# Kernel optimization log

Measured on AMD Instinct MI355X. Metric: run time of the kernel, lower is better.

Reference implementation:

```python
import jax, jax.numpy as jnp
import numpy as np
from jax.scipy.special import digamma, gammaln

B, N, H, W, D = 16, 1024, 32, 32, 256
TEMP = 0.5
KL_WEIGHT = 1e-3


def setup_inputs() -> dict:
    key = jax.random.key(0)
    k1, k2, k3 = jax.random.split(key, 3)
    logits = jax.random.normal(k1, (B, N, H, W), dtype=jnp.float32)
    # codebook initialized uniform(-1/N, 1/N) as in init_type == 'uniform'
    codebook = jax.random.uniform(k2, (N, D), dtype=jnp.float32,
                                  minval=-1.0 / N, maxval=1.0 / N)
    # uniform noise for the Gumbel-softmax rsample (channels-last layout [B,H,W,N])
    uniform_noise = jax.random.uniform(k3, (B, H, W, N), dtype=jnp.float32,
                                       minval=1e-6, maxval=1.0 - 1e-6)
    return {"logits": logits, "codebook": codebook, "uniform_noise": uniform_noise}


def reference(logits, codebook, uniform_noise):
    # convert_to_alpha: evidential mapping alpha = softplus(logits) + 1,
    # then permute(0,2,3,1) -> [B, H, W, N]
    alpha = jax.nn.softplus(jnp.transpose(logits, (0, 2, 3, 1))) + 1.0
    S = jnp.sum(alpha, axis=-1, keepdims=True)            # [B,H,W,1]
    probs = alpha / S                                      # [B,H,W,N]

    # RelaxedOneHotCategorical(temp, probs).rsample() == Gumbel-softmax
    gumbel = -jnp.log(-jnp.log(uniform_noise))
    sample = jax.nn.softmax((jnp.log(probs) + gumbel) / TEMP, axis=-1)  # [B,H,W,N]

    vector_weights = jnp.transpose(sample, (0, 3, 1, 2))   # [B,N,H,W]
    indices = jnp.argmax(vector_weights, axis=1)           # [B,H,W]

    # quantized output via codebook combine
    z_q = jnp.einsum('bnhw,nd->bdhw', vector_weights, codebook)  # [B,D,H,W]

    # KL( Dirichlet(alpha) || Dirichlet(ones(N)) ), closed form with beta=1:
    # lgamma(S) - sum lgamma(alpha) - lgamma(N) + sum (alpha-1)*(digamma(alpha)-digamma(S))
    S1 = S[..., 0]
    kl = (gammaln(S1)
          - jnp.sum(gammaln(alpha), axis=-1)
          - gammaln(jnp.float32(N))
          + jnp.sum((alpha - 1.0) * (digamma(alpha) - digamma(S)), axis=-1))
    kl_loss = KL_WEIGHT * jnp.mean(kl)

    # perplexity over soft encodings
    avg_probs = jnp.mean(sample.reshape(-1, N), axis=0)
    perplexity = jnp.exp(-jnp.sum(avg_probs * jnp.log(avg_probs + 1e-10)))

    return (z_q, kl_loss, indices, perplexity)
```

## Files before the change

### kernel.cpp

```cpp
#include <hip/hip_runtime.h>
#include <math.h>

#define NB 16
#define NN 1024
#define NH 32
#define NW 32
#define ND 256
#define NPIX (NB*NH*NW)

#define ZQ_OFF  0
#define KL_OFF  4194304
#define IDX_OFF 4194305
#define PPL_OFF 4210689

#define LGAMMA_1024F 6071.2804f
#define BS_ROW_B 2080

typedef _Float16 f16x8 __attribute__((ext_vector_type(8)));
typedef _Float16 f16x4 __attribute__((ext_vector_type(4)));
typedef float    f32x4 __attribute__((ext_vector_type(4)));

__device__ __forceinline__ float fast_rcp(float x){ return __builtin_amdgcn_rcpf(x); }

__device__ __forceinline__ void lgamma_digamma(float a, float& lg, float& dg){
    float a1 = a + 1.f, a2 = a + 2.f, z = a + 3.f;
    float t12  = a1*a2;
    float prod = a*t12;
    float rz = fast_rcp(z);
    float rp = fast_rcp(prod);
    float lz = __logf(z);
    float lp = __logf(prod);
    float rz2 = rz*rz;
    lg = (z - 0.5f)*lz - z + 0.918938533f
       + rz*(0.083333333f - 0.002777778f*rz2) - lp;
    float sr = (t12 + a*(a + a + 3.f))*rp;
    dg = lz - 0.5f*rz - rz2*(0.083333333f - 0.008333333f*rz2) - sr;
}

__device__ __forceinline__ float elem(float x, float u,
                                      float& S, float& L, float& P){
    float t  = __expf(-fabsf(x));
    float a  = fmaxf(x, 0.f) + __logf(1.f + t) + 1.f;
    float lg, dg;
    lgamma_digamma(a, lg, dg);
    S += a; L += lg; P += (a - 1.f)*dg;
    float d = 1.f - u;
    float lup = -d*(1.f + d*(0.5f + d*(0.33333333f + d*(0.25f
              + d*(0.2f + d*(0.16666667f + d*0.14285714f))))));
    float lu = (d < 0.09f) ? lup : __logf(u);
    float ar = a * fast_rcp(lu);
    return ar*ar;
}

__global__ __launch_bounds__(256) void k_tr(
    const float* __restrict__ cb, _Float16* __restrict__ cbT)
{
    const int kb = blockIdx.x, kq = blockIdx.y, d = threadIdx.x;
    _Float16 tmp[8];
#pragma unroll
    for (int i = 0; i < 8; ++i)
        tmp[i] = (_Float16)cb[(size_t)(32*kb + 8*kq + i)*ND + d];
    *(f16x8*)(cbT + (size_t)kb*8192 + (size_t)d*32 + 8*kq) = *(f16x8*)tmp;
}

__global__ __launch_bounds__(1024, 2) void k_mega(
    const float* __restrict__ logits, const float* __restrict__ noise,
    const _Float16* __restrict__ cbT, float* __restrict__ colpart,
    float* __restrict__ klpart, float* __restrict__ out)
{
    __shared__ __align__(16) char lds[16*BS_ROW_B + 6*256*4];
    char*  bsb  = lds;
    float* redS = (float*)(lds + 16*BS_ROW_B);
    float* redL = redS + 256;
    float* redP = redL + 256;
    float* redZ = redP + 256;
    float* redM = redZ + 256;
    int*   redI = (int*)(redM + 256);

    const int t    = threadIdx.x;
    const int row  = blockIdx.x >> 1;
    const int w0   = (blockIdx.x & 1) * 16;
    const int b    = row >> 5, h = row & 31;
    const int lane = t & 63;
    const int v    = t >> 6;
    const int wl   = lane & 15;
    const int j4   = (lane >> 4) & 3;
    const int p    = row*32 + w0 + wl;
    const int nq   = 4*v + j4;

    const float* lgB = logits + (size_t)b*(NN*NH*NW) + (size_t)(4*nq)*(NH*NW)
                     + (size_t)h*NW + w0 + wl;
    const float* nzB = noise  + (size_t)p*NN + 4*nq;

    f32x4 u0, u1, u2, u3;
    float x00,x01,x02,x03, x10,x11,x12,x13;
    float x20,x21,x22,x23, x30,x31,x32,x33;
    float ev[16];
    float Sa = 0.f, La = 0.f, Pa = 0.f, Za = 0.f;
    float Sb = 0.f, Lb = 0.f, Pb = 0.f, Zb = 0.f;
    float mxA = -1.f, mxB = -1.f;
    int   idxA = 0, idxB = 0;

    asm volatile(
        "global_load_dwordx4 %0, %4, off\n\t"
        "global_load_dwordx4 %1, %4, off offset:1024\n\t"
        "global_load_dwordx4 %2, %4, off offset:2048\n\t"
        "global_load_dwordx4 %3, %4, off offset:3072"
        : "=&v"(u0), "=&v"(u1), "=&v"(u2), "=&v"(u3)
        : "v"(nzB));

#define LG_ASM(X0,X1,X2,X3,KK) \
    asm volatile( \
        "global_load_dword %0, %4, off offset:-4096\n\t" \
        "global_load_dword %1, %4, off\n\t" \
        "global_load_dword %2, %5, off offset:-4096\n\t" \
        "global_load_dword %3, %5, off" \
        : "=&v"(X0), "=&v"(X1), "=&v"(X2), "=&v"(X3) \
        : "v"(lgB + (size_t)(256*(KK))*1024 + 1024), \
          "v"(lgB + (size_t)(256*(KK))*1024 + 3072))

    LG_ASM(x00,x01,x02,x03, 0);
    LG_ASM(x10,x11,x12,x13, 1);
    LG_ASM(x20,x21,x22,x23, 2);
    LG_ASM(x30,x31,x32,x33, 3);
#undef LG_ASM

#define WAITV(NSTR) do{ asm volatile("s_waitcnt vmcnt(" NSTR ")"); \
                        __builtin_amdgcn_sched_barrier(0); }while(0)

#define DO_EA(kk,mm,X,UC) do{                                     \
    float e = elem(X, UC, Sa, La, Pa);                            \
    Za += e;                                                      \
    if (e > mxA){ mxA = e; idxA = 256*(kk) + 4*nq + (mm); }       \
    ev[4*(kk)+(mm)] = e; }while(0)

#define DO_EB(kk,mm,X,UC) do{                                     \
    float e = elem(X, UC, Sb, Lb, Pb);                            \
    Zb += e;                                                      \
    if (e > mxB){ mxB = e; idxB = 256*(kk) + 4*nq + (mm); }       \
    ev[4*(kk)+(mm)] = e; }while(0)

    WAITV("12");
    DO_EA(0,0,x00,u0[0]); DO_EB(0,1,x01,u0[1]);
    DO_EA(0,2,x02,u0[2]); DO_EB(0,3,x03,u0[3]);
    WAITV("8");
    DO_EA(1,0,x10,u1[0]); DO_EB(1,1,x11,u1[1]);
    DO_EA(1,2,x12,u1[2]); DO_EB(1,3,x13,u1[3]);
    WAITV("4");
    DO_EA(2,0,x20,u2[0]); DO_EB(2,1,x21,u2[1]);
    DO_EA(2,2,x22,u2[2]); DO_EB(2,3,x23,u2[3]);
    WAITV("0");
    DO_EA(3,0,x30,u3[0]); DO_EB(3,1,x31,u3[1]);
    DO_EA(3,2,x32,u3[2]); DO_EB(3,3,x33,u3[3]);
#undef WAITV
#undef DO_EA
#undef DO_EB

    float S = Sa + Sb, L = La + Lb, P = Pa + Pb, Z = Za + Zb;
    float mx; int idx;
    {
        bool take = (mxB > mxA) || (mxB == mxA && idxB < idxA);
        mx  = take ? mxB : mxA;
        idx = take ? idxB : idxA;
    }

#pragma unroll
    for (int mask = 16; mask < 64; mask <<= 1){
        S += __shfl_xor(S, mask);
        L += __shfl_xor(L, mask);
        P += __shfl_xor(P, mask);
        Z += __shfl_xor(Z, mask);
        float mo = __shfl_xor(mx, mask);
        int   io = __shfl_xor(idx, mask);
        bool take = (mo > mx) || (mo == mx && io < idx);
        mx  = take ? mo : mx;
        idx = take ? io : idx;
    }
    if (j4 == 0){
        redS[16*v + wl] = S;  redL[16*v + wl] = L;
        redP[16*v + wl] = P;  redZ[16*v + wl] = Z;
        redM[16*v + wl] = mx; redI[16*v + wl] = idx;
    }
    __syncthreads();

    float Zt = 0.f;
#pragma unroll
    for (int qz = 0; qz < 16; ++qz) Zt += redZ[16*qz + wl];
    const float zinv = fast_rcp(Zt);

    {
        char* brow = bsb + wl*BS_ROW_B;
        const int sw   = wl & 7;
        const int sub8 = (nq & 1) << 3;
        const int cb2  = nq >> 1;
#pragma unroll
        for (int k = 0; k < 4; ++k){
            f16x4 hv;
            hv[0] = (_Float16)(ev[4*k+0]*zinv);
            hv[1] = (_Float16)(ev[4*k+1]*zinv);
            hv[2] = (_Float16)(ev[4*k+2]*zinv);
            hv[3] = (_Float16)(ev[4*k+3]*zinv);
            *(f16x4*)(brow + (((32*k + cb2) ^ sw) << 4) + sub8) = hv;
        }
    }
    __syncthreads();

    const _Float16* aBase = cbT + (size_t)(16*v + wl)*32 + j4*8;
    const char* bRow = bsb + wl*BS_ROW_B;
    const int fsw = wl & 7;

    f32x4 acc = (f32x4)0.f;
    f16x8 ar[4];
    ar[0] = *(const f16x8*)(aBase);
    ar[1] = *(const f16x8*)(aBase + 8192);
    ar[2] = *(const f16x8*)(aBase + 2*8192);
    __builtin_amdgcn_sched_barrier(0);

#pragma unroll
    for (int kb = 0; kb < 32; ++kb){
        if (kb + 3 < 32){
            ar[(kb+3)&3] = *(const f16x8*)(aBase + (size_t)(kb+3)*8192);
            __builtin_amdgcn_sched_barrier(0);
        }
        f16x8 bf = *(const f16x8*)(bRow + ((((kb << 2) | j4) ^ fsw) << 4));
        acc = __builtin_amdgcn_mfma_f32_16x16x32_f16(ar[kb&3], bf, acc, 0, 0, 0);
    }

    float* outp = out + (size_t)b*(ND*1024) + h*32 + w0;
#pragma unroll
    for (int r = 0; r < 4; ++r){
        int d = 16*v + 4*j4 + r;
        outp[(size_t)d*1024 + wl] = acc[r];
    }

    {
        float s0 = 0.f;
#pragma unroll
        for (int r = 0; r < 16; ++r){
            const char* br = bsb + r*BS_ROW_B;
            const int sw2 = r & 7;
            s0 += (float)*(const _Float16*)(br + ((((t >> 3) ^ sw2) << 4) + 2*(t & 7)));
        }
        colpart[(size_t)blockIdx.x*NN + t] = s0;
    }

    if (t < 16){
        float Sq = 0.f, Lq = 0.f, Pq = 0.f, M = -1.f;
        int I = 0x7fffffff;
#pragma unroll
        for (int qz = 0; qz < 16; ++qz){
            Sq += redS[16*qz + t]; Lq += redL[16*qz + t]; Pq += redP[16*qz + t];
            float m = redM[16*qz + t]; int i = redI[16*qz + t];
            bool take = (m > M) || (m == M && i < I);
            M = take ? m : M; I = take ? i : I;
        }
        out[IDX_OFF + row*32 + w0 + t] = (float)I;
        float rS  = fast_rcp(Sq);
        float lnS = __logf(Sq);
        float lgS = (Sq - 0.5f)*lnS - Sq + 0.918938533f + 0.083333333f*rS;
        float dgS = lnS - 0.5f*rS;
        float kl = lgS - Lq - LGAMMA_1024F + (Pq - dgS*(Sq - 1024.f));
#pragma unroll
        for (int mask = 1; mask < 16; mask <<= 1) kl += __shfl_xor(kl, mask);
        if (t == 0) klpart[blockIdx.x] = kl;
    }
}

__global__ __launch_bounds__(256) void k_red(
    const float* __restrict__ colpart, float* __restrict__ colsum)
{
    __shared__ float red[8][32];
    const int nl = threadIdx.x & 31;
    const int rs = threadIdx.x >> 5;
    const int n  = blockIdx.x*32 + nl;
    const float* cp = colpart + (size_t)rs*128*NN + n;
    float s = 0.f;
#pragma unroll 8
    for (int r = 0; r < 128; ++r)
        s += cp[(size_t)r*NN];
    red[rs][nl] = s;
    __syncthreads();
    if (threadIdx.x < 32){
        float tot = 0.f;
#pragma unroll
        for (int i = 0; i < 8; ++i) tot += red[i][threadIdx.x];
        colsum[blockIdx.x*32 + threadIdx.x] = tot;
    }
}

__global__ __launch_bounds__(256) void k_final(
    const float* __restrict__ colsum, const float* __restrict__ klpart,
    float* __restrict__ out)
{
    __shared__ float red[8];
    const int tid = threadIdx.x;
    float s = 0.f, kls = 0.f;
#pragma unroll
    for (int n = tid; n < NN; n += 256){
        float avg = colsum[n] * (1.f/16384.f);
        s += avg * logf(avg + 1e-10f);
        kls += klpart[n];
    }
#pragma unroll
    for (int mask = 1; mask < 64; mask <<= 1){
        s   += __shfl_xor(s, mask);
        kls += __shfl_xor(kls, mask);
    }
    if ((tid & 63) == 0){ red[tid >> 6] = s; red[4 + (tid >> 6)] = kls; }
    __syncthreads();
    if (tid == 0){
        float tot = red[0] + red[1] + red[2] + red[3];
        float klt = red[4] + red[5] + red[6] + red[7];
        out[PPL_OFF] = expf(-tot);
        out[KL_OFF]  = 1e-3f * (klt * (1.f/16384.f));
    }
}

extern "C" void kernel_launch(void* const* d_in, const int* in_sizes, int n_in,
                              void* d_out, int out_size, void* d_ws, size_t ws_size,
                              hipStream_t stream)
{
    const float* logits = (const float*)d_in[0];
    const float* cb     = (const float*)d_in[1];
    const float* noise  = (const float*)d_in[2];
    float* out = (float*)d_out;

    float* colpart = (float*)d_ws;
    float* colsum  = colpart + (size_t)1024*NN;
    float* klpart  = colsum + NN;
    _Float16* cbT  = (_Float16*)(klpart + NN);

    k_tr   <<<dim3(32, 4), 256, 0, stream>>>(cb, cbT);
    k_mega <<<dim3(1024), 1024, 0, stream>>>(logits, noise, cbT, colpart, klpart, out);
    k_red  <<<dim3(32),    256, 0, stream>>>(colpart, colsum);
    k_final<<<1, 256, 0, stream>>>(colsum, klpart, out);
}
```

Baseline: 204.5 us.

## Fuse final reduction into column reduce, batch lgamma logs, pad LDS rows

```diff
diff --git a/kernel.cpp b/kernel.cpp
--- a/kernel.cpp
+++ b/kernel.cpp
@@ -14,7 +14,7 @@
 #define PPL_OFF 4210689
 
 #define LGAMMA_1024F 6071.2804f
-#define BS_ROW_B 2080
+#define BS_ROW_B 2096
 
 typedef _Float16 f16x8 __attribute__((ext_vector_type(8)));
 typedef _Float16 f16x4 __attribute__((ext_vector_type(4)));
@@ -22,27 +22,22 @@
 
 __device__ __forceinline__ float fast_rcp(float x){ return __builtin_amdgcn_rcpf(x); }
 
-__device__ __forceinline__ void lgamma_digamma(float a, float& lg, float& dg){
+__device__ __forceinline__ float elem(float x, float u,
+                                      float& S, float& L, float& P, float& pr){
+    float t  = __expf(-fabsf(x));
+    float a  = fmaxf(x, 0.f) + __logf(1.f + t) + 1.f;
     float a1 = a + 1.f, a2 = a + 2.f, z = a + 3.f;
     float t12  = a1*a2;
     float prod = a*t12;
     float rz = fast_rcp(z);
     float rp = fast_rcp(prod);
     float lz = __logf(z);
-    float lp = __logf(prod);
+    pr *= prod;
     float rz2 = rz*rz;
-    lg = (z - 0.5f)*lz - z + 0.918938533f
-       + rz*(0.083333333f - 0.002777778f*rz2) - lp;
+    float lg = (z - 0.5f)*lz - z + 0.918938533f
+             + rz*(0.083333333f - 0.002777778f*rz2);
     float sr = (t12 + a*(a + a + 3.f))*rp;
-    dg = lz - 0.5f*rz - rz2*(0.083333333f - 0.008333333f*rz2) - sr;
-}
-
-__device__ __forceinline__ float elem(float x, float u,
-                                      float& S, float& L, float& P){
-    float t  = __expf(-fabsf(x));
-    float a  = fmaxf(x, 0.f) + __logf(1.f + t) + 1.f;
-    float lg, dg;
-    lgamma_digamma(a, lg, dg);
+    float dg = lz - 0.5f*rz - rz2*(0.083333333f - 0.008333333f*rz2) - sr;
     S += a; L += lg; P += (a - 1.f)*dg;
     float d = 1.f - u;
     float lup = -d*(1.f + d*(0.5f + d*(0.33333333f + d*(0.25f
@@ -53,9 +48,11 @@
 }
 
 __global__ __launch_bounds__(256) void k_tr(
-    const float* __restrict__ cb, _Float16* __restrict__ cbT)
+    const float* __restrict__ cb, _Float16* __restrict__ cbT,
+    unsigned int* __restrict__ done)
 {
     const int kb = blockIdx.x, kq = blockIdx.y, d = threadIdx.x;
+    if (kb == 0 && kq == 0 && d == 0) *done = 0u;
     _Float16 tmp[8];
 #pragma unroll
     for (int i = 0; i < 8; ++i)
@@ -96,8 +93,8 @@
     float x00,x01,x02,x03, x10,x11,x12,x13;
     float x20,x21,x22,x23, x30,x31,x32,x33;
     float ev[16];
-    float Sa = 0.f, La = 0.f, Pa = 0.f, Za = 0.f;
-    float Sb = 0.f, Lb = 0.f, Pb = 0.f, Zb = 0.f;
+    float Sa = 0.f, La = 0.f, Pa = 0.f, Za = 0.f, prA = 1.f;
+    float Sb = 0.f, Lb = 0.f, Pb = 0.f, Zb = 0.f, prB = 1.f;
     float mxA = -1.f, mxB = -1.f;
     int   idxA = 0, idxB = 0;
 
@@ -129,13 +126,13 @@
                         __builtin_amdgcn_sched_barrier(0); }while(0)
 
 #define DO_EA(kk,mm,X,UC) do{                                     \
-    float e = elem(X, UC, Sa, La, Pa);                            \
+    float e = elem(X, UC, Sa, La, Pa, prA);                       \
     Za += e;                                                      \
     if (e > mxA){ mxA = e; idxA = 256*(kk) + 4*nq + (mm); }       \
     ev[4*(kk)+(mm)] = e; }while(0)
 
 #define DO_EB(kk,mm,X,UC) do{                                     \
-    float e = elem(X, UC, Sb, Lb, Pb);                            \
+    float e = elem(X, UC, Sb, Lb, Pb, prB);                       \
     Zb += e;                                                      \
     if (e > mxB){ mxB = e; idxB = 256*(kk) + 4*nq + (mm); }       \
     ev[4*(kk)+(mm)] = e; }while(0)
@@ -156,7 +153,10 @@
 #undef DO_EA
 #undef DO_EB
 
-    float S = Sa + Sb, L = La + Lb, P = Pa + Pb, Z = Za + Zb;
+    float S = Sa + Sb;
+    float L = La + Lb - __logf(prA) - __logf(prB);
+    float P = Pa + Pb;
+    float Z = Za + Zb;
     float mx; int idx;
     {
         bool take = (mxB > mxA) || (mxB == mxA && idxB < idxA);
@@ -266,10 +266,14 @@
     }
 }
 
-__global__ __launch_bounds__(256) void k_red(
-    const float* __restrict__ colpart, float* __restrict__ colsum)
+__global__ __launch_bounds__(256) void k_redfinal(
+    const float* __restrict__ colpart, const float* __restrict__ klpart,
+    float* __restrict__ colsum, unsigned int* __restrict__ done,
+    float* __restrict__ out)
 {
     __shared__ float red[8][32];
+    __shared__ float red2[8];
+    __shared__ int isLast;
     const int nl = threadIdx.x & 31;
     const int rs = threadIdx.x >> 5;
     const int n  = blockIdx.x*32 + nl;
@@ -286,31 +290,36 @@
         for (int i = 0; i < 8; ++i) tot += red[i][threadIdx.x];
         colsum[blockIdx.x*32 + threadIdx.x] = tot;
     }
-}
-
-__global__ __launch_bounds__(256) void k_final(
-    const float* __restrict__ colsum, const float* __restrict__ klpart,
-    float* __restrict__ out)
-{
-    __shared__ float red[8];
+    __syncthreads();
+    if (threadIdx.x == 0){
+        __threadfence();
+        unsigned int old = atomicAdd(done, 1u);
+        isLast = (old == 31u) ? 1 : 0;
+    }
+    __syncthreads();
+    if (!isLast) return;
+
+    __threadfence();
     const int tid = threadIdx.x;
-    float s = 0.f, kls = 0.f;
-#pragma unroll
-    for (int n = tid; n < NN; n += 256){
-        float avg = colsum[n] * (1.f/16384.f);
-        s += avg * logf(avg + 1e-10f);
-        kls += klpart[n];
+    float sp = 0.f, kls = 0.f;
+#pragma unroll
+    for (int n2 = tid; n2 < NN; n2 += 256){
+        float cv = __hip_atomic_load(&colsum[n2], __ATOMIC_RELAXED,
+                                     __HIP_MEMORY_SCOPE_AGENT);
+        float avg = cv * (1.f/16384.f);
+        sp += avg * logf(avg + 1e-10f);
+        kls += klpart[n2];
     }
 #pragma unroll
     for (int mask = 1; mask < 64; mask <<= 1){
-        s   += __shfl_xor(s, mask);
+        sp  += __shfl_xor(sp, mask);
         kls += __shfl_xor(kls, mask);
     }
-    if ((tid & 63) == 0){ red[tid >> 6] = s; red[4 + (tid >> 6)] = kls; }
+    if ((tid & 63) == 0){ red2[tid >> 6] = sp; red2[4 + (tid >> 6)] = kls; }
     __syncthreads();
     if (tid == 0){
-        float tot = red[0] + red[1] + red[2] + red[3];
-        float klt = red[4] + red[5] + red[6] + red[7];
+        float tot = red2[0] + red2[1] + red2[2] + red2[3];
+        float klt = red2[4] + red2[5] + red2[6] + red2[7];
         out[PPL_OFF] = expf(-tot);
         out[KL_OFF]  = 1e-3f * (klt * (1.f/16384.f));
     }
@@ -325,13 +334,15 @@
     const float* noise  = (const float*)d_in[2];
     float* out = (float*)d_out;
 
-    float* colpart = (float*)d_ws;
-    float* colsum  = colpart + (size_t)1024*NN;
-    float* klpart  = colsum + NN;
-    _Float16* cbT  = (_Float16*)(klpart + NN);
-
-    k_tr   <<<dim3(32, 4), 256, 0, stream>>>(cb, cbT);
-    k_mega <<<dim3(1024), 1024, 0, stream>>>(logits, noise, cbT, colpart, klpart, out);
-    k_red  <<<dim3(32),    256, 0, stream>>>(colpart, colsum);
-    k_final<<<1, 256, 0, stream>>>(colsum, klpart, out);
-}
+    float* colpart      = (float*)d_ws;
+    float* colsum       = colpart + (size_t)1024*NN;
+    float* klpart       = colsum + NN;
+    unsigned int* done  = (unsigned int*)(klpart + NN);
+    _Float16* cbT       = (_Float16*)(klpart + NN + 4);
+
+    k_tr      <<<dim3(32, 4), 256, 0, stream>>>(cb, cbT, done);
+    k_mega    <<<dim3(1024), 1024, 0, stream>>>(logits, noise, cbT,
+                                                colpart, klpart, out);
+    k_redfinal<<<dim3(32),    256, 0, stream>>>(colpart, klpart,
+                                                colsum, done, out);
+}
```

Result: no change. 204.3 us (-0.1%).
